# Optimization experiments

Measured on AMD Instinct MI355X. Metric: run time of the kernel, lower is better.

## Reference

```python
import jax, jax.numpy as jnp
import numpy as np

BN_EPS = 1e-5
HEADS = 8

def _bn(y, gamma, beta, mean, var):
    # eval-mode BatchNorm2d over channel axis 1; y: [B,C,H,W]
    scale = gamma / jnp.sqrt(var + BN_EPS)
    shift = beta - mean * scale
    return y * scale[None, :, None, None] + shift[None, :, None, None]

def setup_inputs() -> dict:
    key = jax.random.key(0)
    ks = jax.random.split(key, 12)
    B, C, H, W = 16, 256, 64, 64
    x = jax.random.normal(ks[0], (B, C, H, W), jnp.float32)
    qkv_w = jax.random.normal(ks[1], (3 * C, C), jnp.float32) * 0.05
    qkv_gamma = jax.random.uniform(ks[2], (3 * C,), jnp.float32, 0.5, 1.5)
    qkv_beta = jax.random.normal(ks[3], (3 * C,), jnp.float32) * 0.1
    qkv_mean = jax.random.normal(ks[4], (3 * C,), jnp.float32) * 0.1
    qkv_var = jax.random.uniform(ks[5], (3 * C,), jnp.float32, 0.5, 1.5)
    proj_w = jax.random.normal(ks[6], (C, C), jnp.float32) * 0.05
    proj_gamma = jax.random.uniform(ks[7], (C,), jnp.float32, 0.5, 1.5)
    proj_beta = jax.random.normal(ks[8], (C,), jnp.float32) * 0.1
    proj_mean = jax.random.normal(ks[9], (C,), jnp.float32) * 0.1
    proj_var = jax.random.uniform(ks[10], (C,), jnp.float32, 0.5, 1.5)
    return {"x": x, "qkv_w": qkv_w, "qkv_gamma": qkv_gamma, "qkv_beta": qkv_beta,
            "qkv_mean": qkv_mean, "qkv_var": qkv_var, "proj_w": proj_w,
            "proj_gamma": proj_gamma, "proj_beta": proj_beta,
            "proj_mean": proj_mean, "proj_var": proj_var}

def reference(x, qkv_w, qkv_gamma, qkv_beta, qkv_mean, qkv_var,
              proj_w, proj_gamma, proj_beta, proj_mean, proj_var):
    B, C, H, W = x.shape
    hd = C // HEADS  # head_dim
    # 1x1 conv (no bias) + BN
    qkv = jnp.einsum('bchw,oc->bohw', x, qkv_w)
    qkv = _bn(qkv, qkv_gamma, qkv_beta, qkv_mean, qkv_var)
    q, k, v = jnp.split(qkv, 3, axis=1)
    N = H * W
    q = q.reshape(B, HEADS, hd, N)
    k = k.reshape(B, HEADS, hd, N)
    v = v.reshape(B, HEADS, hd, N)
    q = jax.nn.softmax(q, axis=-1)   # over tokens
    k = jax.nn.softmax(k, axis=-2)   # over head_dim
    context = jnp.einsum('bhdn,bhen->bhde', k, v)   # [B,h,d,d]
    out = jnp.einsum('bhdn,bhde->bhen', q, context) # [B,h,d,N]
    out = out.reshape(B, C, H, W)
    out = jnp.einsum('bchw,oc->bohw', out, proj_w)
    out = _bn(out, proj_gamma, proj_beta, proj_mean, proj_var)
    return out
```

## Files before the change

### kernel.cpp

```cpp
#include <hip/hip_runtime.h>

typedef unsigned short ushort_t;
typedef unsigned int u32;
typedef short short8 __attribute__((ext_vector_type(8)));
typedef float f32x4 __attribute__((ext_vector_type(4)));
typedef float f32x16 __attribute__((ext_vector_type(16)));

#define NTOK 4096
#define NCOLS 65536
#define CIN 256

__device__ __forceinline__ float b2f(ushort_t u) {
    union { unsigned int i; float f; } v; v.i = ((unsigned int)u) << 16; return v.f;
}
__device__ __forceinline__ ushort_t f2b(float f) {
    union { float f; unsigned int i; } v; v.f = f;
    unsigned int r = v.i + 0x7FFFu + ((v.i >> 16) & 1u);
    return (ushort_t)(r >> 16);
}

__device__ __forceinline__ void gl_lds16(const ushort_t* g, ushort_t* l) {
    __builtin_amdgcn_global_load_lds(
        (const __attribute__((address_space(1))) u32*)(const void*)g,
        (__attribute__((address_space(3))) u32*)(void*)l,
        16, 0, 0);
}

__global__ __launch_bounds__(256) void prep_x(const float* __restrict__ x,
                                              ushort_t* __restrict__ xt,
                                              const float* __restrict__ wq,
                                              const float* __restrict__ wp,
                                              ushort_t* __restrict__ wqb,
                                              ushort_t* __restrict__ wpb) {
    __shared__ ushort_t lds[64 * 264];
    int tid = threadIdx.x;

    int i = blockIdx.x * 256 + tid;
    if (i < 768 * 256) wqb[i] = f2b(wq[i]);
    else               wpb[i - 768 * 256] = f2b(wp[i - 768 * 256]);

    int g0 = blockIdx.x * 64;
    int b = g0 >> 12, n0 = g0 & 4095;
    const float* src = x + (size_t)b * (CIN * NTOK);
    int tn = tid & 63, cg = tid >> 6;
    for (int c4 = 0; c4 < 64; c4++) {
        int c = c4 * 4 + cg;
        lds[tn * 264 + c] = f2b(src[(size_t)c * NTOK + n0 + tn]);
    }
    __syncthreads();
    int tok = tid >> 2, c8 = (tid & 3) * 8;
    ushort_t* dst = xt + (size_t)(g0 + tok) * CIN + c8;
#pragma unroll
    for (int j = 0; j < 8; j++)
        *(short8*)(dst + j * 32) = *(const short8*)&lds[tok * 264 + c8 + j * 32];
}

__global__ __launch_bounds__(256) void gemm128(const ushort_t* __restrict__ W,
                                               const ushort_t* __restrict__ Xc,
                                               const float* __restrict__ gamma,
                                               const float* __restrict__ beta,
                                               const float* __restrict__ mean,
                                               const float* __restrict__ var,
                                               ushort_t* __restrict__ out_b,
                                               float* __restrict__ out_f,
                                               int mtiles, int mode) {
    __shared__ __align__(16) ushort_t lA[128 * 32];
    __shared__ __align__(16) ushort_t lB[128 * 32];
    int tid = threadIdx.x;
    int wave = tid >> 6, lane = tid & 63;
    int l15 = lane & 15, q = lane >> 4;
    int mh = wave >> 1, nh = wave & 1;

    int bid = blockIdx.x;
    int swz = (bid & 7) * (mtiles * 64) + (bid >> 3);
    int m0 = (swz % mtiles) * 128, colb = (swz / mtiles) * 128;

    f32x4 acc[4][4];
#pragma unroll
    for (int i = 0; i < 4; i++)
#pragma unroll
        for (int j = 0; j < 4; j++)
#pragma unroll
            for (int r = 0; r < 4; r++) acc[i][j][r] = 0.f;

    const ushort_t* gA0 = W  + (size_t)(m0 +      (tid >> 2)) * CIN + (tid & 3) * 8;
    const ushort_t* gA1 = W  + (size_t)(m0 + 64 + (tid >> 2)) * CIN + (tid & 3) * 8;
    const ushort_t* gB0 = Xc + (size_t)(colb +      (tid >> 2)) * CIN + (tid & 3) * 8;
    const ushort_t* gB1 = Xc + (size_t)(colb + 64 + (tid >> 2)) * CIN + (tid & 3) * 8;
    ushort_t* la0 = &lA[tid * 8];
    ushort_t* la1 = &lA[2048 + tid * 8];
    ushort_t* lb0 = &lB[tid * 8];
    ushort_t* lb1 = &lB[2048 + tid * 8];

    for (int k0 = 0; k0 < CIN; k0 += 32) {
        gl_lds16(gA0 + k0, la0);
        gl_lds16(gA1 + k0, la1);
        gl_lds16(gB0 + k0, lb0);
        gl_lds16(gB1 + k0, lb1);
        __syncthreads();
        short8 af[4], bf[4];
#pragma unroll
        for (int i = 0; i < 4; i++) {
            af[i] = *(const short8*)&lA[(mh * 64 + i * 16 + l15) * 32 + q * 8];
            bf[i] = *(const short8*)&lB[(nh * 64 + i * 16 + l15) * 32 + q * 8];
        }
#pragma unroll
        for (int mi = 0; mi < 4; mi++)
#pragma unroll
            for (int ni = 0; ni < 4; ni++)
                acc[mi][ni] = __builtin_amdgcn_mfma_f32_16x16x32_bf16(af[mi], bf[ni],
                                                                      acc[mi][ni], 0, 0, 0);
        __syncthreads();
    }

    int col_l = colb + nh * 64 + l15;
#pragma unroll
    for (int mi = 0; mi < 4; mi++) {
#pragma unroll
        for (int r = 0; r < 4; r++) {
            int m = m0 + mh * 64 + mi * 16 + q * 4 + r;
            float sc = gamma[m] * rsqrtf(var[m] + 1e-5f);
            float sh = beta[m] - mean[m] * sc;
#pragma unroll
            for (int ni = 0; ni < 4; ni++) {
                float val = acc[mi][ni][r] * sc + sh;
                int col = col_l + ni * 16;
                if (mode == 0) {
                    out_b[(size_t)m * NCOLS + col] = f2b(val);
                } else {
                    int bb = col >> 12, n = col & 4095;
                    out_f[(size_t)bb * (CIN * NTOK) + (size_t)m * NTOK + n] = val;
                }
            }
        }
    }
}

__global__ __launch_bounds__(256) void sum_ker(const ushort_t* __restrict__ qkv,
                                               float* __restrict__ qsums,
                                               float* __restrict__ rsums) {
    int tid = threadIdx.x;
    if (blockIdx.x < 1024) {
        int wave = tid >> 6, lane = tid & 63;
        int rid = blockIdx.x * 4 + wave;
        int c = rid >> 4, b = rid & 15;
        const ushort_t* row = qkv + (size_t)c * NCOLS + b * NTOK;
        float s = 0.f;
#pragma unroll
        for (int j = 0; j < 8; j++) {
            short8 pk = *(const short8*)(row + j * 512 + lane * 8);
#pragma unroll
            for (int i = 0; i < 8; i++) s += __expf(b2f((ushort_t)pk[i]));
        }
        for (int off = 1; off < 64; off <<= 1) s += __shfl_xor(s, off);
        if (lane == 0) qsums[c * 16 + b] = s;
    } else {
        int kb = blockIdx.x - 1024;
        int bh = kb >> 1, half = kb & 1;
        int b = bh >> 3, h = bh & 7;
        const ushort_t* base = qkv + (size_t)(256 + h * 32) * NCOLS
                                   + b * NTOK + half * 2048 + tid * 8;
        float s[8];
#pragma unroll
        for (int j = 0; j < 8; j++) s[j] = 0.f;
        for (int ch = 0; ch < 32; ch++) {
            short8 kk = *(const short8*)(base + (size_t)ch * NCOLS);
#pragma unroll
            for (int j = 0; j < 8; j++) s[j] += __expf(b2f((ushort_t)kk[j]));
        }
        float* rp = rsums + (size_t)bh * NTOK + half * 2048 + tid * 8;
        f32x4 r0, r1;
#pragma unroll
        for (int j = 0; j < 4; j++) { r0[j] = 1.f / s[j]; r1[j] = 1.f / s[j + 4]; }
        *(f32x4*)rp = r0;
        *(f32x4*)(rp + 4) = r1;
    }
}

__global__ __launch_bounds__(256) void ctx_ker(const ushort_t* __restrict__ qkv,
                                               const float* __restrict__ rsums,
                                               float* __restrict__ ctxpart) {
    int sl = blockIdx.x, bh = blockIdx.y;
    int b = bh >> 3, h = bh & 7;
    int tid = threadIdx.x, wave = tid >> 6, lane = tid & 63;
    int l31 = lane & 31, l5 = lane >> 5;
    int col0 = b * NTOK + sl * 512 + wave * 128;
    const ushort_t* krow = qkv + (size_t)(256 + h * 32 + l31) * NCOLS + col0 + l5 * 8;
    const ushort_t* vrow = qkv + (size_t)(512 + h * 32 + l31) * NCOLS + col0 + l5 * 8;
    const float* rsp = rsums + (size_t)bh * NTOK + sl * 512 + wave * 128 + l5 * 8;
    f32x16 acc;
#pragma unroll
    for (int i = 0; i < 16; i++) acc[i] = 0.f;
#pragma unroll
    for (int st = 0; st < 8; st++) {
        short8 kf = *(const short8*)(krow + st * 16);
        short8 vf = *(const short8*)(vrow + st * 16);
        f32x4 ra = *(const f32x4*)(rsp + st * 16);
        f32x4 rb = *(const f32x4*)(rsp + st * 16 + 4);
        short8 af;
#pragma unroll
        for (int j = 0; j < 4; j++)
            af[j] = (short)f2b(__expf(b2f((ushort_t)kf[j])) * ra[j]);
#pragma unroll
        for (int j = 0; j < 4; j++)
            af[j + 4] = (short)f2b(__expf(b2f((ushort_t)kf[j + 4])) * rb[j]);
        acc = __builtin_amdgcn_mfma_f32_32x32x16_bf16(af, vf, acc, 0, 0, 0);
    }
    __shared__ float red[4][1024];
#pragma unroll
    for (int r = 0; r < 16; r++) {
        int d = (r & 3) + 8 * (r >> 2) + 4 * l5;
        red[wave][d * 32 + l31] = acc[r];
    }
    __syncthreads();
    int i0 = tid * 4;
    f32x4 vv;
#pragma unroll
    for (int i = 0; i < 4; i++)
        vv[i] = red[0][i0 + i] + red[1][i0 + i] + red[2][i0 + i] + red[3][i0 + i];
    *(f32x4*)(ctxpart + ((size_t)sl * 128 + bh) * 1024 + i0) = vv;
}

__global__ __launch_bounds__(256) void out_ker(const ushort_t* __restrict__ qkv,
                                               const float* __restrict__ ctxpart,
                                               const float* __restrict__ qsums,
                                               ushort_t* __restrict__ attT) {
    int sl = blockIdx.x, bh = blockIdx.y;
    int b = bh >> 3, h = bh & 7;
    int tid = threadIdx.x, wave = tid >> 6, lane = tid & 63;
    int l31 = lane & 31, l5 = lane >> 5;
    __shared__ __align__(16) ushort_t ctxT[32 * 40];
    __shared__ __align__(16) ushort_t qT[256 * 40];
    __shared__ __align__(16) ushort_t obuf[4][32 * 40];

    {
        int i0 = tid * 4;
        f32x4 v;
#pragma unroll
        for (int i = 0; i < 4; i++) v[i] = 0.f;
#pragma unroll
        for (int s = 0; s < 8; s++)
            v += *(const f32x4*)(ctxpart + ((size_t)s * 128 + bh) * 1024 + i0);
#pragma unroll
        for (int i = 0; i < 4; i++) {
            int idx = i0 + i;
            int d = idx >> 5, e = idx & 31;
            ctxT[e * 40 + d] = f2b(v[i]);
        }
    }
    __syncthreads();
    short8 a0 = *(const short8*)(ctxT + l31 * 40 + l5 * 8);
    short8 a1 = *(const short8*)(ctxT + l31 * 40 + 16 + l5 * 8);

    const ushort_t* qbase = qkv + (size_t)(h * 32) * NCOLS;
    int segbase = b * NTOK + sl * 512;
    int d = tid & 31, t8 = (tid >> 5) * 8;
    float sq = 1.f / qsums[(h * 32 + d) * 16 + b];

    for (int nc = 0; nc < 2; nc++) {
        int gcol0 = segbase + nc * 256;
#pragma unroll
        for (int jj = 0; jj < 4; jj++) {
            int tok8 = jj * 64 + t8;
            short8 pk = *(const short8*)(qbase + (size_t)d * NCOLS + gcol0 + tok8);
#pragma unroll
            for (int j = 0; j < 8; j++)
                qT[(tok8 + j) * 40 + d] = f2b(__expf(b2f((ushort_t)pk[j])) * sq);
        }
        __syncthreads();
#pragma unroll
        for (int ti = 0; ti < 2; ti++) {
            int tok0 = (wave + ti * 4) * 32;
            f32x16 acc;
#pragma unroll
            for (int i = 0; i < 16; i++) acc[i] = 0.f;
            short8 b0 = *(const short8*)(qT + (size_t)(tok0 + l31) * 40 + l5 * 8);
            short8 b1 = *(const short8*)(qT + (size_t)(tok0 + l31) * 40 + 16 + l5 * 8);
            acc = __builtin_amdgcn_mfma_f32_32x32x16_bf16(a0, b0, acc, 0, 0, 0);
            acc = __builtin_amdgcn_mfma_f32_32x32x16_bf16(a1, b1, acc, 0, 0, 0);
#pragma unroll
            for (int r = 0; r < 16; r++) {
                int e = (r & 3) + 8 * (r >> 2) + 4 * l5;
                obuf[wave][l31 * 40 + e] = f2b(acc[r]);
            }
            {
                int tok = lane >> 1, half = lane & 1;
                const ushort_t* srcp = &obuf[wave][tok * 40 + half * 16];
                short8 r0 = *(const short8*)srcp;
                short8 r1 = *(const short8*)(srcp + 8);
                size_t g = (size_t)(gcol0 + tok0 + tok) * 256 + h * 32 + half * 16;
                *(short8*)(attT + g) = r0;
                *(short8*)(attT + g + 8) = r1;
            }
        }
        __syncthreads();
    }
}

extern "C" void kernel_launch(void* const* d_in, const int* in_sizes, int n_in,
                              void* d_out, int out_size, void* d_ws, size_t ws_size,
                              hipStream_t stream) {
    const float* x          = (const float*)d_in[0];
    const float* qkv_w      = (const float*)d_in[1];
    const float* qkv_gamma  = (const float*)d_in[2];
    const float* qkv_beta   = (const float*)d_in[3];
    const float* qkv_mean   = (const float*)d_in[4];
    const float* qkv_var    = (const float*)d_in[5];
    const float* proj_w     = (const float*)d_in[6];
    const float* proj_gamma = (const float*)d_in[7];
    const float* proj_beta  = (const float*)d_in[8];
    const float* proj_mean  = (const float*)d_in[9];
    const float* proj_var   = (const float*)d_in[10];

    ushort_t* wqb = (ushort_t*)d_ws;
    ushort_t* wpb = wqb + 768 * 256;
    ushort_t* xt  = wpb + 256 * 256;
    ushort_t* qkv = xt + (size_t)NCOLS * CIN;
    float* out     = (float*)d_out;
    float* ctxpart = (float*)d_out;
    float* rsums   = ctxpart + 8 * 128 * 1024;
    float* qsums   = rsums + 128 * NTOK;

    prep_x<<<1024, 256, 0, stream>>>(x, xt, qkv_w, proj_w, wqb, wpb);
    gemm128<<<3072, 256, 0, stream>>>(wqb, xt, qkv_gamma, qkv_beta,
                                      qkv_mean, qkv_var, qkv, nullptr, 6, 0);
    sum_ker<<<1280, 256, 0, stream>>>(qkv, qsums, rsums);
    ctx_ker<<<dim3(8, 128), 256, 0, stream>>>(qkv, rsums, ctxpart);
    out_ker<<<dim3(8, 128), 256, 0, stream>>>(qkv, ctxpart, qsums, xt);
    gemm128<<<1024, 256, 0, stream>>>(wpb, xt, proj_gamma, proj_beta,
                                      proj_mean, proj_var, nullptr, out, 2, 1);
}
```

Before: 281.2 us.

## Fuse softmax sum kernel into ctx kernel and XOR-swizzle GEMM LDS reads

Removes the separate sum_ker launch. The per-token k softmax denominators are now computed inside ctx_ker and kept in shared memory. Partial q row sums are written per slice and reduced in out_ker, which avoids a full extra pass over q and k and the global rsums buffer. Separately, the GEMM's global-to-LDS loads and fragment reads use an XOR swizzle on the 16-byte chunk index to reduce LDS bank conflicts. ctx_ker gains an extra k/q read phase and a barrier before its MFMA loop.

```diff
diff --git a/kernel.cpp b/kernel.cpp
--- a/kernel.cpp
+++ b/kernel.cpp
@@ -83,14 +83,17 @@
 #pragma unroll
             for (int r = 0; r < 4; r++) acc[i][j][r] = 0.f;
 
-    const ushort_t* gA0 = W  + (size_t)(m0 +      (tid >> 2)) * CIN + (tid & 3) * 8;
-    const ushort_t* gA1 = W  + (size_t)(m0 + 64 + (tid >> 2)) * CIN + (tid & 3) * 8;
-    const ushort_t* gB0 = Xc + (size_t)(colb +      (tid >> 2)) * CIN + (tid & 3) * 8;
-    const ushort_t* gB1 = Xc + (size_t)(colb + 64 + (tid >> 2)) * CIN + (tid & 3) * 8;
+    int xoff = (((tid & 3) ^ ((tid >> 2) & 3)) * 8);
+    const ushort_t* gA0 = W  + (size_t)(m0 +      (tid >> 2)) * CIN + xoff;
+    const ushort_t* gA1 = W  + (size_t)(m0 + 64 + (tid >> 2)) * CIN + xoff;
+    const ushort_t* gB0 = Xc + (size_t)(colb +      (tid >> 2)) * CIN + xoff;
+    const ushort_t* gB1 = Xc + (size_t)(colb + 64 + (tid >> 2)) * CIN + xoff;
     ushort_t* la0 = &lA[tid * 8];
     ushort_t* la1 = &lA[2048 + tid * 8];
     ushort_t* lb0 = &lB[tid * 8];
     ushort_t* lb1 = &lB[2048 + tid * 8];
+
+    int qa = (q ^ (l15 & 3)) * 8;
 
     for (int k0 = 0; k0 < CIN; k0 += 32) {
         gl_lds16(gA0 + k0, la0);
@@ -101,8 +104,8 @@
         short8 af[4], bf[4];
 #pragma unroll
         for (int i = 0; i < 4; i++) {
-            af[i] = *(const short8*)&lA[(mh * 64 + i * 16 + l15) * 32 + q * 8];
-            bf[i] = *(const short8*)&lB[(nh * 64 + i * 16 + l15) * 32 + q * 8];
+            af[i] = *(const short8*)&lA[(mh * 64 + i * 16 + l15) * 32 + qa];
+            bf[i] = *(const short8*)&lB[(nh * 64 + i * 16 + l15) * 32 + qa];
         }
 #pragma unroll
         for (int mi = 0; mi < 4; mi++)
@@ -136,58 +139,54 @@
     }
 }
 
-__global__ __launch_bounds__(256) void sum_ker(const ushort_t* __restrict__ qkv,
-                                               float* __restrict__ qsums,
-                                               float* __restrict__ rsums) {
-    int tid = threadIdx.x;
-    if (blockIdx.x < 1024) {
-        int wave = tid >> 6, lane = tid & 63;
-        int rid = blockIdx.x * 4 + wave;
-        int c = rid >> 4, b = rid & 15;
-        const ushort_t* row = qkv + (size_t)c * NCOLS + b * NTOK;
-        float s = 0.f;
-#pragma unroll
-        for (int j = 0; j < 8; j++) {
-            short8 pk = *(const short8*)(row + j * 512 + lane * 8);
-#pragma unroll
-            for (int i = 0; i < 8; i++) s += __expf(b2f((ushort_t)pk[i]));
-        }
-        for (int off = 1; off < 64; off <<= 1) s += __shfl_xor(s, off);
-        if (lane == 0) qsums[c * 16 + b] = s;
-    } else {
-        int kb = blockIdx.x - 1024;
-        int bh = kb >> 1, half = kb & 1;
-        int b = bh >> 3, h = bh & 7;
-        const ushort_t* base = qkv + (size_t)(256 + h * 32) * NCOLS
-                                   + b * NTOK + half * 2048 + tid * 8;
-        float s[8];
-#pragma unroll
-        for (int j = 0; j < 8; j++) s[j] = 0.f;
-        for (int ch = 0; ch < 32; ch++) {
-            short8 kk = *(const short8*)(base + (size_t)ch * NCOLS);
-#pragma unroll
-            for (int j = 0; j < 8; j++) s[j] += __expf(b2f((ushort_t)kk[j]));
-        }
-        float* rp = rsums + (size_t)bh * NTOK + half * 2048 + tid * 8;
-        f32x4 r0, r1;
-#pragma unroll
-        for (int j = 0; j < 4; j++) { r0[j] = 1.f / s[j]; r1[j] = 1.f / s[j + 4]; }
-        *(f32x4*)rp = r0;
-        *(f32x4*)(rp + 4) = r1;
-    }
-}
-
 __global__ __launch_bounds__(256) void ctx_ker(const ushort_t* __restrict__ qkv,
-                                               const float* __restrict__ rsums,
-                                               float* __restrict__ ctxpart) {
+                                               float* __restrict__ ctxpart,
+                                               float* __restrict__ qpart) {
     int sl = blockIdx.x, bh = blockIdx.y;
     int b = bh >> 3, h = bh & 7;
     int tid = threadIdx.x, wave = tid >> 6, lane = tid & 63;
     int l31 = lane & 31, l5 = lane >> 5;
-    int col0 = b * NTOK + sl * 512 + wave * 128;
+    int colbase = b * NTOK + sl * 512;
+
+    __shared__ float rsm[512];
+    __shared__ float red2[256];
+
+    {
+        const ushort_t* kb = qkv + (size_t)(256 + h * 32) * NCOLS + colbase + tid * 2;
+        float s0 = 0.f, s1 = 0.f;
+#pragma unroll
+        for (int d = 0; d < 32; d++) {
+            u32 w = *(const u32*)(kb + (size_t)d * NCOLS);
+            s0 += __expf(b2f((ushort_t)(w & 0xffffu)));
+            s1 += __expf(b2f((ushort_t)(w >> 16)));
+        }
+        rsm[tid * 2]     = 1.f / s0;
+        rsm[tid * 2 + 1] = 1.f / s1;
+    }
+    {
+        int ch = tid >> 3, slot = tid & 7;
+        const ushort_t* qb = qkv + (size_t)(h * 32 + ch) * NCOLS + colbase + slot * 64;
+        float s = 0.f;
+#pragma unroll
+        for (int j = 0; j < 8; j++) {
+            short8 pk = *(const short8*)(qb + j * 8);
+#pragma unroll
+            for (int i = 0; i < 8; i++) s += __expf(b2f((ushort_t)pk[i]));
+        }
+        red2[tid] = s;
+    }
+    __syncthreads();
+    if (tid < 32) {
+        float ss = 0.f;
+#pragma unroll
+        for (int k = 0; k < 8; k++) ss += red2[tid * 8 + k];
+        qpart[((size_t)sl * 128 + bh) * 32 + tid] = ss;
+    }
+
+    int col0 = colbase + wave * 128;
     const ushort_t* krow = qkv + (size_t)(256 + h * 32 + l31) * NCOLS + col0 + l5 * 8;
     const ushort_t* vrow = qkv + (size_t)(512 + h * 32 + l31) * NCOLS + col0 + l5 * 8;
-    const float* rsp = rsums + (size_t)bh * NTOK + sl * 512 + wave * 128 + l5 * 8;
+    int rbase = wave * 128 + l5 * 8;
     f32x16 acc;
 #pragma unroll
     for (int i = 0; i < 16; i++) acc[i] = 0.f;
@@ -195,8 +194,8 @@
     for (int st = 0; st < 8; st++) {
         short8 kf = *(const short8*)(krow + st * 16);
         short8 vf = *(const short8*)(vrow + st * 16);
-        f32x4 ra = *(const f32x4*)(rsp + st * 16);
-        f32x4 rb = *(const f32x4*)(rsp + st * 16 + 4);
+        f32x4 ra = *(const f32x4*)&rsm[rbase + st * 16];
+        f32x4 rb = *(const f32x4*)&rsm[rbase + st * 16 + 4];
         short8 af;
 #pragma unroll
         for (int j = 0; j < 4; j++)
@@ -223,7 +222,7 @@
 
 __global__ __launch_bounds__(256) void out_ker(const ushort_t* __restrict__ qkv,
                                                const float* __restrict__ ctxpart,
-                                               const float* __restrict__ qsums,
+                                               const float* __restrict__ qpart,
                                                ushort_t* __restrict__ attT) {
     int sl = blockIdx.x, bh = blockIdx.y;
     int b = bh >> 3, h = bh & 7;
@@ -255,7 +254,10 @@
     const ushort_t* qbase = qkv + (size_t)(h * 32) * NCOLS;
     int segbase = b * NTOK + sl * 512;
     int d = tid & 31, t8 = (tid >> 5) * 8;
-    float sq = 1.f / qsums[(h * 32 + d) * 16 + b];
+    float ssum = 0.f;
+#pragma unroll
+    for (int s = 0; s < 8; s++) ssum += qpart[((size_t)s * 128 + bh) * 32 + d];
+    float sq = 1.f / ssum;
 
     for (int nc = 0; nc < 2; nc++) {
         int gcol0 = segbase + nc * 256;
@@ -318,15 +320,13 @@
     ushort_t* qkv = xt + (size_t)NCOLS * CIN;
     float* out     = (float*)d_out;
     float* ctxpart = (float*)d_out;
-    float* rsums   = ctxpart + 8 * 128 * 1024;
-    float* qsums   = rsums + 128 * NTOK;
+    float* qpart   = ctxpart + 8 * 128 * 1024;
 
     prep_x<<<1024, 256, 0, stream>>>(x, xt, qkv_w, proj_w, wqb, wpb);
     gemm128<<<3072, 256, 0, stream>>>(wqb, xt, qkv_gamma, qkv_beta,
                                       qkv_mean, qkv_var, qkv, nullptr, 6, 0);
-    sum_ker<<<1280, 256, 0, stream>>>(qkv, qsums, rsums);
-    ctx_ker<<<dim3(8, 128), 256, 0, stream>>>(qkv, rsums, ctxpart);
-    out_ker<<<dim3(8, 128), 256, 0, stream>>>(qkv, ctxpart, qsums, xt);
+    ctx_ker<<<dim3(8, 128), 256, 0, stream>>>(qkv, ctxpart, qpart);
+    out_ker<<<dim3(8, 128), 256, 0, stream>>>(qkv, ctxpart, qpart, xt);
     gemm128<<<1024, 256, 0, stream>>>(wpb, xt, proj_gamma, proj_beta,
                                       proj_mean, proj_var, nullptr, out, 2, 1);
 }
```

Result: faster. 263.5 us (-6.3%).
